# Performance work log

Measured on AMD Instinct MI355X. Metric: run time of the kernel, lower is better.

The kernel has to match this reference:

```python
import jax, jax.numpy as jnp
import numpy as np

K = 3        # kernel_size
PAD = 1      # padding ('same' for stride 1)
RANK = 53    # CP rank from compression=10: round(27*32*64/(10*(9+32+64)))


def _kaiming_uniform(key, shape, fan_in):
    # matches nn.init.kaiming_uniform_(a=sqrt(5)): bound = 1/sqrt(fan_in)
    bound = 1.0 / np.sqrt(fan_in)
    return jax.random.uniform(key, shape, jnp.float32, -bound, bound)


def setup_inputs() -> dict:
    key = jax.random.key(0)
    ks = jax.random.split(key, 7)
    B, Cin, Cout, H, W, D = 1, 32, 64, 56, 56, 56
    x = jax.random.normal(ks[0], (B, Cin, H, W, D), jnp.float32)
    # CP factor matrices (fan_in = second dim for torch's 2D kaiming)
    U_kh = _kaiming_uniform(ks[1], (K, RANK), RANK)
    U_kw = _kaiming_uniform(ks[2], (K, RANK), RANK)
    U_kd = _kaiming_uniform(ks[3], (K, RANK), RANK)
    U_cin = _kaiming_uniform(ks[4], (Cin, RANK), RANK)
    U_cout = _kaiming_uniform(ks[5], (RANK, Cout), Cout)
    bias = jax.random.normal(ks[6], (Cout,), jnp.float32)
    return {"x": x, "U_kh": U_kh, "U_kw": U_kw, "U_kd": U_kd,
            "U_cin": U_cin, "U_cout": U_cout, "bias": bias}


def reference(x, U_kh, U_kw, U_kd, U_cin, U_cout, bias):
    B, C, H, W, D = x.shape
    xp = jnp.pad(x, ((0, 0), (0, 0), (PAD, PAD), (PAD, PAD), (PAD, PAD)))
    # im2col patches: patches[i,j,l,b,c,x,y,z] = xp[b,c,x+i,y+j,z+l]
    # (same values/ordering as torch unfold(2).unfold(3).unfold(4), stride=1)
    patches = jnp.stack([
        xp[:, :, i:i + H, j:j + W, l:l + D]
        for i in range(K) for j in range(K) for l in range(K)
    ]).reshape(K, K, K, B, C, H, W, D)
    # CP tensor-network contraction (legs: k_h,k_w,k_d,c_in share rank r -> c_out)
    out = jnp.einsum('ijlbcxyz,ir,jr,lr,cr,ro->boxyz',
                     patches, U_kh, U_kw, U_kd, U_cin, U_cout,
                     optimize=True)
    return out + bias[None, :, None, None, None]
```

## Files before the change

### kernel.cpp

```cpp
#include <hip/hip_runtime.h>


#define NP 175616
#define NQ 43904
#define HSTR 3136
#define CIN 32
#define RK 53
#define COUT 64
#define SCR 53

__global__ __launch_bounds__(256) void k0_t(const float* __restrict__ Ucin,
                                            float* __restrict__ Ut)
{
    int t = blockIdx.x * 256 + threadIdx.x;
    if (t < RK * CIN) {
        int r = t >> 5, c = t & 31;
        Ut[t] = Ucin[c * RK + r];
    }
}

__global__ __launch_bounds__(256) void k1f4(
    const float4* __restrict__ x4, const float* __restrict__ Ut,
    float4* __restrict__ T1)
{
    const int q = blockIdx.x * 256 + threadIdx.x;
    if (q >= NQ) return;
    float4 xv[CIN];
#pragma unroll
    for (int c = 0; c < CIN; ++c) xv[c] = x4[(size_t)c * NQ + q];
#pragma unroll 2
    for (int r = 0; r < RK; ++r) {
        const float* U = Ut + r * CIN;
        float4 a; a.x = 0.f; a.y = 0.f; a.z = 0.f; a.w = 0.f;
#pragma unroll
        for (int c = 0; c < CIN; ++c) {
            float u = U[c];
            a.x += xv[c].x * u; a.y += xv[c].y * u;
            a.z += xv[c].z * u; a.w += xv[c].w * u;
        }
        T1[(size_t)r * NQ + q] = a;
    }
}

__global__ __launch_bounds__(256) void k2a(
    float* T1, const float* __restrict__ Ukw, const float* __restrict__ Ukd)
{
    __shared__ float sIn[56 * 58];
    __shared__ float sA [58 * 56];
    const int h = blockIdx.x;
    const int r = blockIdx.y;
    const int tid = threadIdx.x;
    const float kd0 = Ukd[r], kd1 = Ukd[RK + r], kd2 = Ukd[2 * RK + r];
    const float kw0 = Ukw[r], kw1 = Ukw[RK + r], kw2 = Ukw[2 * RK + r];
    float* P = T1 + (size_t)r * NP + h * HSTR;

    for (int t = tid; t < 112; t += 256) {
        int i = t >> 1;
        if (t & 1) { sIn[i * 58] = 0.f; sIn[i * 58 + 57] = 0.f; }
        else       { sA[i] = 0.f;       sA[57 * 56 + i] = 0.f; }
    }
    for (int idx = tid; idx < 3136; idx += 256) {
        int w = idx / 56, d = idx - w * 56;
        sIn[w * 58 + d + 1] = P[idx];
    }
    __syncthreads();
    for (int idx = tid; idx < 3136; idx += 256) {
        int w = idx / 56, d = idx - w * 56;
        const float* b = &sIn[w * 58 + d];
        sA[(w + 1) * 56 + d] = b[0] * kd0 + b[1] * kd1 + b[2] * kd2;
    }
    __syncthreads();
    for (int idx = tid; idx < 3136; idx += 256) {
        const float* a = &sA[idx];
        P[idx] = a[0] * kw0 + a[56] * kw1 + a[112] * kw2;
    }
}

__global__ __launch_bounds__(256) void k3b(
    const float4* __restrict__ Ta, const float* __restrict__ Ucout,
    const float* __restrict__ bias, const float* __restrict__ Ukh,
    float4* __restrict__ Out)
{
    const int lane = threadIdx.x & 63;
    int og = (threadIdx.x >> 6) << 4;
    og = __builtin_amdgcn_readfirstlane(og);
    const int q = blockIdx.x * 64 + lane;
    const int h = q / 784;
    const bool hm = (h > 0), hp = (h < 55);

    float4 a[16];
#pragma unroll
    for (int o = 0; o < 16; ++o) {
        float b = bias[og + o];
        a[o].x = b; a[o].y = b; a[o].z = b; a[o].w = b;
    }
#pragma unroll 2
    for (int r = 0; r < RK; ++r) {
        const float4* S = Ta + (size_t)r * NQ + q;
        const float k0 = Ukh[r], k1 = Ukh[RK + r], k2 = Ukh[2 * RK + r];
        float4 B = S[0];
        float4 A; A.x = 0.f; A.y = 0.f; A.z = 0.f; A.w = 0.f;
        float4 C = A;
        if (hm) A = S[-784];
        if (hp) C = S[784];
        float4 t;
        t.x = A.x * k0 + B.x * k1 + C.x * k2;
        t.y = A.y * k0 + B.y * k1 + C.y * k2;
        t.z = A.z * k0 + B.z * k1 + C.z * k2;
        t.w = A.w * k0 + B.w * k1 + C.w * k2;
        const float* Ur = Ucout + r * COUT + og;
#pragma unroll
        for (int o = 0; o < 16; ++o) {
            float u = Ur[o];
            a[o].x += t.x * u; a[o].y += t.y * u;
            a[o].z += t.z * u; a[o].w += t.w * u;
        }
    }
#pragma unroll
    for (int o = 0; o < 16; ++o)
        Out[(size_t)(og + o) * NQ + q] = a[o];
}


__global__ __launch_bounds__(256) void k1_chunk(
    const float* __restrict__ x, const float* __restrict__ Ucin,
    float* T, int r0, int nr)
{
    __shared__ float sU[11 * CIN];
    const int tid = threadIdx.x;
    for (int t = tid; t < nr * CIN; t += 256) {
        int lr = t >> 5, c = t & 31;
        sU[t] = Ucin[c * RK + (r0 + lr)];
    }
    __syncthreads();
    const int p = blockIdx.x * 256 + tid;
    float xv[CIN];
#pragma unroll
    for (int c = 0; c < CIN; ++c) xv[c] = x[c * NP + p];
#pragma unroll 1
    for (int lr = 0; lr < nr; ++lr) {
        float acc = 0.f;
#pragma unroll
        for (int c = 0; c < CIN; ++c) acc += xv[c] * sU[lr * CIN + c];
        T[(size_t)(SCR + lr) * NP + p] = acc;
    }
}

__global__ __launch_bounds__(256) void k2_chunk(
    const float* __restrict__ Ukh, const float* __restrict__ Ukw,
    const float* __restrict__ Ukd, float* T, int r0)
{
    __shared__ float sIn[5800];
    __shared__ float sA[5600];
    const int lr = blockIdx.z;
    const int r  = r0 + lr;
    const int h0 = blockIdx.x * 8, w0 = blockIdx.y * 8;
    const int tid = threadIdx.x;
    const float kh0 = Ukh[r], kh1 = Ukh[RK + r], kh2 = Ukh[2 * RK + r];
    const float kw0 = Ukw[r], kw1 = Ukw[RK + r], kw2 = Ukw[2 * RK + r];
    const float kd0 = Ukd[r], kd1 = Ukd[RK + r], kd2 = Ukd[2 * RK + r];
    const float* T1r = T + (size_t)(SCR + lr) * NP;

    for (int idx = tid; idx < 5800; idx += 256) {
        int d = idx % 58; int t2 = idx / 58; int ww = t2 % 10; int hh = t2 / 10;
        int gh = h0 + hh - 1, gw = w0 + ww - 1, gd = d - 1;
        float v = 0.f;
        if ((unsigned)gh < 56u && (unsigned)gw < 56u && (unsigned)gd < 56u)
            v = T1r[gh * HSTR + gw * 56 + gd];
        sIn[idx] = v;
    }
    __syncthreads();
    for (int idx = tid; idx < 5600; idx += 256) {
        int d = idx % 56; int t2 = idx / 56; int ww = t2 % 10; int hh = t2 / 10;
        const float* b = &sIn[(hh * 10 + ww) * 58 + d];
        sA[idx] = b[0] * kd0 + b[1] * kd1 + b[2] * kd2;
    }
    __syncthreads();
    const float k00 = kh0 * kw0, k01 = kh0 * kw1, k02 = kh0 * kw2;
    const float k10 = kh1 * kw0, k11 = kh1 * kw1, k12 = kh1 * kw2;
    const float k20 = kh2 * kw0, k21 = kh2 * kw1, k22 = kh2 * kw2;
    for (int idx = tid; idx < 3584; idx += 256) {
        int d = idx % 56; int t2 = idx / 56; int ww = t2 % 8; int hh = t2 / 8;
        const float* a = &sA[(hh * 10 + ww) * 56 + d];
        float acc = a[0]    * k00 + a[56]   * k01 + a[112]  * k02
                  + a[560]  * k10 + a[616]  * k11 + a[672]  * k12
                  + a[1120] * k20 + a[1176] * k21 + a[1232] * k22;
        T[(size_t)r * NP + (h0 + hh) * HSTR + (w0 + ww) * 56 + d] = acc;
    }
}

__global__ __launch_bounds__(256) void k3_out(
    float* T, const float* __restrict__ Ucout, const float* __restrict__ bias)
{
    __shared__ float sUo[RK * COUT];
    __shared__ float sB[COUT];
    const int tid = threadIdx.x;
    for (int t = tid; t < RK * COUT; t += 256) sUo[t] = Ucout[t];
    if (tid < COUT) sB[tid] = bias[tid];
    __syncthreads();
    const int p = blockIdx.x * 256 + tid;
    float acc[COUT];
#pragma unroll
    for (int o = 0; o < COUT; ++o) acc[o] = sB[o];
#pragma unroll 1
    for (int r = 0; r < RK; ++r) {
        float t = T[(size_t)r * NP + p];
        const float* Ur = &sUo[r * COUT];
#pragma unroll
        for (int o = 0; o < COUT; ++o) acc[o] += t * Ur[o];
    }
#pragma unroll
    for (int o = 0; o < COUT; ++o) T[(size_t)o * NP + p] = acc[o];
}


extern "C" void kernel_launch(void* const* d_in, const int* in_sizes, int n_in,
                              void* d_out, int out_size, void* d_ws, size_t ws_size,
                              hipStream_t stream)
{
    const float* x     = (const float*)d_in[0];
    const float* Ukh   = (const float*)d_in[1];
    const float* Ukw   = (const float*)d_in[2];
    const float* Ukd   = (const float*)d_in[3];
    const float* Ucin  = (const float*)d_in[4];
    const float* Ucout = (const float*)d_in[5];
    const float* bias  = (const float*)d_in[6];

    const size_t t1_bytes = (size_t)RK * NP * sizeof(float);

    if (ws_size >= t1_bytes) {
        float* T1 = (float*)d_ws;
        float* Ut = (float*)d_out;
        k0_t<<<7, 256, 0, stream>>>(Ucin, Ut);
        k1f4<<<(NQ + 255) / 256, 256, 0, stream>>>((const float4*)x, Ut, (float4*)T1);
        k2a<<<dim3(56, RK), 256, 0, stream>>>(T1, Ukw, Ukd);
        k3b<<<NQ / 64, 256, 0, stream>>>((const float4*)T1, Ucout, bias, Ukh,
                                         (float4*)d_out);
    } else {
        float* T = (float*)d_out;
        for (int r0 = 0; r0 < RK; r0 += 11) {
            int nr = (RK - r0 < 11) ? (RK - r0) : 11;
            k1_chunk<<<NP / 256, 256, 0, stream>>>(x, Ucin, T, r0, nr);
            k2_chunk<<<dim3(7, 7, nr), 256, 0, stream>>>(Ukh, Ukw, Ukd, T, r0);
        }
        k3_out<<<NP / 256, 256, 0, stream>>>(T, Ucout, bias);
    }
}
```

Measured before the change: 174.1 us.

## Rework T1 projection to scalar per-point, vectorize W/D stencil, bound k3 occupancy

The first projection kernel now gives each thread one point instead of four, which cuts register use and launches four times as many threads. The W/D separable stencil pass now uses float4 shared-memory accesses with explicit boundary handling, replacing the padded scalar layout. The output kernel gets a launch-bounds occupancy hint. The transposed U_cin scratch moves from the output buffer into workspace, so the fast path now needs slightly more workspace. The trade-off is higher thread-level parallelism against fewer loads per thread and possible register spills in k3n.

Result: no change. 173.2 us (-0.5%).

```diff
diff --git a/kernel.cpp b/kernel.cpp
--- a/kernel.cpp
+++ b/kernel.cpp
@@ -4,6 +4,7 @@
 #define NP 175616
 #define NQ 43904
 #define HSTR 3136
+#define QH 784
 #define CIN 32
 #define RK 53
 #define COUT 64
@@ -19,64 +20,72 @@
     }
 }
 
-__global__ __launch_bounds__(256) void k1f4(
-    const float4* __restrict__ x4, const float* __restrict__ Ut,
-    float4* __restrict__ T1)
-{
-    const int q = blockIdx.x * 256 + threadIdx.x;
-    if (q >= NQ) return;
-    float4 xv[CIN];
-#pragma unroll
-    for (int c = 0; c < CIN; ++c) xv[c] = x4[(size_t)c * NQ + q];
+__global__ __launch_bounds__(256) void k1n(
+    const float* __restrict__ x, const float* __restrict__ Ut,
+    float* __restrict__ T1)
+{
+    const int p = blockIdx.x * 256 + threadIdx.x;
+    float xv[CIN];
+#pragma unroll
+    for (int c = 0; c < CIN; ++c) xv[c] = x[c * NP + p];
 #pragma unroll 2
     for (int r = 0; r < RK; ++r) {
         const float* U = Ut + r * CIN;
-        float4 a; a.x = 0.f; a.y = 0.f; a.z = 0.f; a.w = 0.f;
-#pragma unroll
-        for (int c = 0; c < CIN; ++c) {
-            float u = U[c];
-            a.x += xv[c].x * u; a.y += xv[c].y * u;
-            a.z += xv[c].z * u; a.w += xv[c].w * u;
-        }
-        T1[(size_t)r * NQ + q] = a;
-    }
-}
-
-__global__ __launch_bounds__(256) void k2a(
+        float acc = 0.f;
+#pragma unroll
+        for (int c = 0; c < CIN; ++c) acc += xv[c] * U[c];
+        T1[(size_t)r * NP + p] = acc;
+    }
+}
+
+__global__ __launch_bounds__(256) void k2n(
     float* T1, const float* __restrict__ Ukw, const float* __restrict__ Ukd)
 {
-    __shared__ float sIn[56 * 58];
-    __shared__ float sA [58 * 56];
+    __shared__ float sIn[3136];
+    __shared__ float sA[3136];
     const int h = blockIdx.x;
     const int r = blockIdx.y;
     const int tid = threadIdx.x;
     const float kd0 = Ukd[r], kd1 = Ukd[RK + r], kd2 = Ukd[2 * RK + r];
     const float kw0 = Ukw[r], kw1 = Ukw[RK + r], kw2 = Ukw[2 * RK + r];
-    float* P = T1 + (size_t)r * NP + h * HSTR;
-
-    for (int t = tid; t < 112; t += 256) {
-        int i = t >> 1;
-        if (t & 1) { sIn[i * 58] = 0.f; sIn[i * 58 + 57] = 0.f; }
-        else       { sA[i] = 0.f;       sA[57 * 56 + i] = 0.f; }
-    }
-    for (int idx = tid; idx < 3136; idx += 256) {
-        int w = idx / 56, d = idx - w * 56;
-        sIn[w * 58 + d + 1] = P[idx];
-    }
-    __syncthreads();
-    for (int idx = tid; idx < 3136; idx += 256) {
-        int w = idx / 56, d = idx - w * 56;
-        const float* b = &sIn[w * 58 + d];
-        sA[(w + 1) * 56 + d] = b[0] * kd0 + b[1] * kd1 + b[2] * kd2;
-    }
-    __syncthreads();
-    for (int idx = tid; idx < 3136; idx += 256) {
-        const float* a = &sA[idx];
-        P[idx] = a[0] * kw0 + a[56] * kw1 + a[112] * kw2;
-    }
-}
-
-__global__ __launch_bounds__(256) void k3b(
+    float4* P4 = (float4*)(T1 + (size_t)r * NP + h * HSTR);
+
+    for (int i = tid; i < QH; i += 256)
+        ((float4*)sIn)[i] = P4[i];
+    __syncthreads();
+
+    for (int i = tid; i < QH; i += 256) {
+        int w = i / 14, d0 = (i - w * 14) * 4;
+        const float* b = &sIn[w * 56 + d0];
+        float4 c = *(const float4*)b;
+        float lm = (d0 > 0)  ? b[-1] : 0.f;
+        float rp = (d0 < 52) ? b[4]  : 0.f;
+        float4 o;
+        o.x = lm  * kd0 + c.x * kd1 + c.y * kd2;
+        o.y = c.x * kd0 + c.y * kd1 + c.z * kd2;
+        o.z = c.y * kd0 + c.z * kd1 + c.w * kd2;
+        o.w = c.z * kd0 + c.w * kd1 + rp  * kd2;
+        ((float4*)sA)[i] = o;
+    }
+    __syncthreads();
+
+    for (int i = tid; i < QH; i += 256) {
+        int w = i / 14;
+        float4 m = ((const float4*)sA)[i];
+        float4 a0, a2;
+        a0.x = a0.y = a0.z = a0.w = 0.f; a2 = a0;
+        if (w > 0)  a0 = ((const float4*)sA)[i - 14];
+        if (w < 55) a2 = ((const float4*)sA)[i + 14];
+        float4 res;
+        res.x = a0.x * kw0 + m.x * kw1 + a2.x * kw2;
+        res.y = a0.y * kw0 + m.y * kw1 + a2.y * kw2;
+        res.z = a0.z * kw0 + m.z * kw1 + a2.z * kw2;
+        res.w = a0.w * kw0 + m.w * kw1 + a2.w * kw2;
+        P4[i] = res;
+    }
+}
+
+__global__ __launch_bounds__(256, 4) void k3n(
     const float4* __restrict__ Ta, const float* __restrict__ Ucout,
     const float* __restrict__ bias, const float* __restrict__ Ukh,
     float4* __restrict__ Out)
@@ -85,7 +94,7 @@
     int og = (threadIdx.x >> 6) << 4;
     og = __builtin_amdgcn_readfirstlane(og);
     const int q = blockIdx.x * 64 + lane;
-    const int h = q / 784;
+    const int h = q / QH;
     const bool hm = (h > 0), hp = (h < 55);
 
     float4 a[16];
@@ -101,8 +110,8 @@
         float4 B = S[0];
         float4 A; A.x = 0.f; A.y = 0.f; A.z = 0.f; A.w = 0.f;
         float4 C = A;
-        if (hm) A = S[-784];
-        if (hp) C = S[784];
+        if (hm) A = S[-QH];
+        if (hp) C = S[QH];
         float4 t;
         t.x = A.x * k0 + B.x * k1 + C.x * k2;
         t.y = A.y * k0 + B.y * k1 + C.y * k2;
@@ -228,13 +237,13 @@
 
     const size_t t1_bytes = (size_t)RK * NP * sizeof(float);
 
-    if (ws_size >= t1_bytes) {
+    if (ws_size >= t1_bytes + 8192) {
         float* T1 = (float*)d_ws;
-        float* Ut = (float*)d_out;
+        float* Ut = (float*)((char*)d_ws + t1_bytes);
         k0_t<<<7, 256, 0, stream>>>(Ucin, Ut);
-        k1f4<<<(NQ + 255) / 256, 256, 0, stream>>>((const float4*)x, Ut, (float4*)T1);
-        k2a<<<dim3(56, RK), 256, 0, stream>>>(T1, Ukw, Ukd);
-        k3b<<<NQ / 64, 256, 0, stream>>>((const float4*)T1, Ucout, bias, Ukh,
+        k1n<<<NP / 256, 256, 0, stream>>>(x, Ut, T1);
+        k2n<<<dim3(56, RK), 256, 0, stream>>>(T1, Ukw, Ukd);
+        k3n<<<NQ / 64, 256, 0, stream>>>((const float4*)T1, Ucout, bias, Ukh,
                                          (float4*)d_out);
     } else {
         float* T = (float*)d_out;
```
